# Kernel optimization log

Measured on AMD Instinct MI355X. Metric: run time of the kernel, lower is better.

The kernel has to match this reference:

```python
import jax, jax.numpy as jnp
import numpy as np

C_V, C_F, C_D = 10, 64, 16
COSTS = jnp.array([10.0, 5.0, 2.0], dtype=jnp.float32)  # bandwidth cost per granularity
PENALTY = 0.0  # no_transmission_utility_penalty


def setup_inputs() -> dict:
    key = jax.random.key(0)
    k1, k2 = jax.random.split(key)
    B, H, W = 4, 192, 192
    collab = jax.random.normal(k1, (B, C_V + C_F + C_D, H, W), dtype=jnp.float32)
    utility = jax.random.normal(k2, (B, H, W, 3), dtype=jnp.float32)
    return {"collab_bev_data_list": collab, "utility_map_list": utility,
            "bandwidth_budget": 200000}


def _selection_mechanism(utility, budget_per_sample):
    # utility: [B, H, W, G]; returns [B, H, W] float selected granularity (-1 = none)
    B, H, W, G = utility.shape
    best_u = jnp.max(utility, axis=3)                      # [B,H,W]
    best_g = jnp.argmax(utility, axis=3)                   # [B,H,W]
    N = B * H * W
    flat_u = best_u.reshape(N)
    flat_g = best_g.reshape(N)
    b_idx = jnp.repeat(jnp.arange(B, dtype=jnp.int32), H * W)
    valid = flat_u > PENALTY
    cost = COSTS[flat_g]                                   # [N]
    # sort candidates by utility, descending (stable, matching list.sort)
    order = jnp.argsort(-flat_u)
    v_s = valid[order]
    c_s = cost[order]
    b_s = b_idx[order]

    # greedy budget-constrained selection per sample (sequential knapsack)
    def step(usage, item):
        v, c, b = item
        ok = v & (usage[b] + c <= budget_per_sample)
        usage = usage.at[b].add(jnp.where(ok, c, jnp.float32(0)))
        return usage, ok

    _, sel_sorted = jax.lax.scan(step, jnp.zeros((B,), jnp.float32), (v_s, c_s, b_s))
    selected = jnp.zeros((N,), bool).at[order].set(sel_sorted)
    idx = jnp.where(selected, flat_g.astype(jnp.float32), jnp.float32(-1.0))
    return idx.reshape(B, H, W)


def _build_sparse_bev(sel_idx, vox, feat, det):
    m0 = (sel_idx == 0.0)[:, None, :, :]
    m1 = (sel_idx == 1.0)[:, None, :, :]
    m2 = (sel_idx == 2.0)[:, None, :, :]
    return jnp.concatenate([vox * m0, feat * m1, det * m2], axis=1)


def reference(collab_bev_data_list, utility_map_list, bandwidth_budget):
    cav_num = collab_bev_data_list.shape[0]
    budget_per_sample = jnp.float32(bandwidth_budget / cav_num)
    sel_idx = _selection_mechanism(utility_map_list, budget_per_sample)
    vox = collab_bev_data_list[:, :C_V]
    feat = collab_bev_data_list[:, C_V:C_V + C_F]
    det = collab_bev_data_list[:, C_V + C_F:C_V + C_F + C_D]
    sparse = _build_sparse_bev(sel_idx, vox, feat, det)
    return sparse, sel_idx
```

## Files before the change

kernel.cpp:

```cpp
#include <hip/hip_runtime.h>
#include <stdint.h>
#include <math.h>

#define B_    4
#define H_    192
#define W_    192
#define HW    (H_*W_)
#define NPIX  (B_*HW)
#define C_V   10
#define C_F   64
#define C_D   16
#define C_ALL (C_V+C_F+C_D)
#define HBINS 32768
#define CAP   2048

#define OFF_HIST 0u
#define OFF_KEY  (4u*HBINS*4u)
#define OFF_G    (OFF_KEY + (uint32_t)NPIX*4u)
#define OFF_SELX (OFF_G + (uint32_t)NPIX)
#define OFF_HL   (OFF_SELX + (uint32_t)NPIX)

__device__ __forceinline__ uint32_t costOf(uint32_t g) {
    return g == 0u ? 10u : (g == 1u ? 5u : 2u);
}

__device__ __forceinline__ uint32_t budgetInt(const int* bptr) {
    double bps = (double)bptr[0] / (double)B_;
    float f = (float)bps;
    return (uint32_t)floorf(f);
}

__global__ void k_zero(uint4* __restrict__ hist4) {
    int i = blockIdx.x * blockDim.x + threadIdx.x;
    hist4[i] = make_uint4(0u, 0u, 0u, 0u);
}

__global__ void k_prep(const float* __restrict__ util, uint4* __restrict__ key4,
                       uint32_t* __restrict__ g4, uint32_t* __restrict__ selx4,
                       uint32_t* __restrict__ hist) {
    int t = blockIdx.x * blockDim.x + threadIdx.x;
    if (t >= NPIX / 4) return;
    const float4* u4 = (const float4*)util + (size_t)t * 3;
    float4 a = u4[0], b4 = u4[1], c4 = u4[2];
    float u[4][3] = { {a.x, a.y, a.z}, {a.w, b4.x, b4.y},
                      {b4.z, b4.w, c4.x}, {c4.y, c4.z, c4.w} };
    uint32_t kk[4]; uint32_t gpack = 0;
    #pragma unroll
    for (int p = 0; p < 4; ++p) {
        float best = u[p][0]; uint32_t g = 0;
        if (u[p][1] > best) { best = u[p][1]; g = 1; }
        if (u[p][2] > best) { best = u[p][2]; g = 2; }
        kk[p] = (best > 0.0f) ? (__float_as_uint(best) | 0x80000000u) : 0u;
        gpack |= g << (8 * p);
    }
    key4[t] = make_uint4(kk[0], kk[1], kk[2], kk[3]);
    g4[t] = gpack;
    selx4[t] = 0u;
    int b = (t * 4) / HW;
    #pragma unroll
    for (int p = 0; p < 4; ++p)
        if (kk[p])
            atomicAdd(&hist[(size_t)b * HBINS + ((kk[p] >> 16) & 32767u)],
                      costOf((gpack >> (8 * p)) & 3u));
}

__global__ __launch_bounds__(1024) void k_select(const uint32_t* __restrict__ key,
                                                 const uint8_t* __restrict__ g,
                                                 const uint32_t* __restrict__ hist,
                                                 const int* __restrict__ budget_ptr,
                                                 uint8_t* __restrict__ selx,
                                                 uint32_t* __restrict__ hl_out) {
    int b = blockIdx.x;
    int t = threadIdx.x;
    uint32_t budget = budgetInt(budget_ptr);

    __shared__ uint32_t scan[1024];
    __shared__ uint64_t e[CAP];
    __shared__ uint64_t s[CAP];
    __shared__ uint64_t red[1024];
    __shared__ uint32_t f_b2, f_usage, sh_n, sh_r, sh_poskey, sh_pospix;

    if (t == 0) { f_b2 = 0xFFFFFFFFu; f_usage = 0u; sh_n = 0u; }
    __syncthreads();

    const uint32_t* hb = hist + (size_t)b * HBINS;
    int hi = 32767 - 32 * t;
    uint32_t cs = 0;
    #pragma unroll 4
    for (int j = 0; j < 32; ++j) cs += hb[hi - j];
    scan[t] = cs;
    __syncthreads();
    for (int off = 1; off < 1024; off <<= 1) {
        uint32_t v = (t >= off) ? scan[t - off] : 0u;
        __syncthreads();
        scan[t] += v;
        __syncthreads();
    }
    uint32_t incl = scan[t], excl = incl - cs;
    if (excl <= budget && incl > budget) {
        uint32_t cum = excl;
        for (int j = 0; j < 32; ++j) {
            uint32_t hv = hb[hi - j];
            if (cum + hv > budget) { f_b2 = (uint32_t)(hi - j); f_usage = cum; break; }
            cum += hv;
        }
    }
    __syncthreads();
    uint32_t b2 = f_b2;
    if (t == 0) {
        uint32_t hl;
        if (b2 == 0xFFFFFFFFu)           hl = 1u;
        else {
            uint32_t bs = b2 + 32768u;
            hl = (bs >= 65535u) ? 0xFFFFFFFFu : ((bs + 1u) << 16);
        }
        hl_out[b] = hl;
    }
    if (b2 == 0xFFFFFFFFu) return;

    const uint32_t* kb = key + (size_t)b * HW;
    const uint8_t*  gb = g   + (size_t)b * HW;
    for (int i = t; i < HW; i += 1024) {
        uint32_t k = kb[i];
        if (k && ((k >> 16) & 32767u) == b2) {
            uint32_t idx = atomicAdd(&sh_n, 1u);
            if (idx < CAP)
                e[idx] = ((uint64_t)(~k) << 32) | ((uint64_t)i << 2) | (uint64_t)gb[i];
        }
    }
    __syncthreads();
    int n = (int)(sh_n < (uint32_t)CAP ? sh_n : (uint32_t)CAP);

    for (int i = t; i < n; i += 1024) {
        uint64_t ei = e[i];
        int rk = 0;
        for (int j = 0; j < n; ++j) rk += (e[j] < ei);
        s[rk] = ei;
    }
    __syncthreads();

    if (t == 0) {
        uint32_t usage = f_usage;
        uint8_t* sx = selx + (size_t)b * HW;
        for (int i = 0; i < n; ++i) {
            uint64_t ei = s[i];
            uint32_t c = costOf((uint32_t)(ei & 3u));
            if (usage + c <= budget) { usage += c; sx[(ei >> 2) & 0xFFFFu] = 1; }
        }
        sh_r = budget - usage;
        sh_poskey = (b2 + 32768u) << 16;
        sh_pospix = 0xFFFFFFFFu;
    }
    __syncthreads();

    for (int round = 0; round < 8; ++round) {
        uint32_t r = sh_r;
        if (r < 2u) break;
        uint32_t pkey = sh_poskey, ppix = sh_pospix;
        uint64_t best = 0;
        for (int i = t; i < HW; i += 1024) {
            uint32_t k = kb[i];
            if (!k) continue;
            if (!(k < pkey || (k == pkey && (uint32_t)i > ppix))) continue;
            if (costOf(gb[i]) > r) continue;
            uint64_t m = ((uint64_t)k << 16) | (uint64_t)(65535u - (uint32_t)i);
            if (m > best) best = m;
        }
        red[t] = best;
        __syncthreads();
        for (int off = 512; off > 0; off >>= 1) {
            if (t < off) {
                uint64_t o = red[t + off];
                if (o > red[t]) red[t] = o;
            }
            __syncthreads();
        }
        if (t == 0) {
            uint64_t m = red[0];
            if (m == 0) sh_r = 0;
            else {
                uint32_t pix = 65535u - (uint32_t)(m & 0xFFFFu);
                uint32_t k   = (uint32_t)(m >> 16);
                uint32_t c   = costOf(gb[pix]);
                selx[(size_t)b * HW + pix] = 1;
                sh_r -= c;
                sh_poskey = k; sh_pospix = pix;
            }
        }
        __syncthreads();
    }
}

__global__ void k_sparse(const float* __restrict__ collab, const uint4* __restrict__ key4,
                         const uint32_t* __restrict__ g4, const uint32_t* __restrict__ selx4,
                         const uint32_t* __restrict__ hl_arr,
                         float* __restrict__ out, float* __restrict__ selOut) {
    int tid = blockIdx.x * blockDim.x + threadIdx.x;
    int c = blockIdx.y, b = blockIdx.z;
    int cls = (c < C_V) ? 0 : ((c < C_V + C_F) ? 1 : 2);
    uint32_t hl = hl_arr[b];
    size_t p4 = (size_t)b * (HW / 4) + (size_t)tid;
    uint4 kk = key4[p4];
    uint32_t gg = g4[p4];
    uint32_t sx = selx4[p4];
    int sc[4];
    uint32_t kv[4] = { kk.x, kk.y, kk.z, kk.w };
    #pragma unroll
    for (int p = 0; p < 4; ++p) {
        bool se = (kv[p] >= hl) || (((sx >> (8 * p)) & 0xFFu) != 0u);
        sc[p] = se ? (int)((gg >> (8 * p)) & 3u) : -1;
    }
    size_t co = ((size_t)(b * C_ALL + c)) * HW + (size_t)tid * 4;
    float4 v = *(const float4*)(collab + co);
    float4 o;
    o.x = (sc[0] == cls) ? v.x : 0.0f;
    o.y = (sc[1] == cls) ? v.y : 0.0f;
    o.z = (sc[2] == cls) ? v.z : 0.0f;
    o.w = (sc[3] == cls) ? v.w : 0.0f;
    *(float4*)(out + co) = o;
    if (c == 0) {
        float4 sf = make_float4((float)sc[0], (float)sc[1], (float)sc[2], (float)sc[3]);
        ((float4*)selOut)[p4] = sf;
    }
}

extern "C" void kernel_launch(void* const* d_in, const int* in_sizes, int n_in,
                              void* d_out, int out_size, void* d_ws, size_t ws_size,
                              hipStream_t stream) {
    (void)in_sizes; (void)n_in; (void)out_size; (void)ws_size;
    const float* collab = (const float*)d_in[0];
    const float* util   = (const float*)d_in[1];
    const int*   budget = (const int*)d_in[2];

    uint8_t*  ws   = (uint8_t*)d_ws;
    uint32_t* hist = (uint32_t*)(ws + OFF_HIST);
    uint32_t* key  = (uint32_t*)(ws + OFF_KEY);
    uint8_t*  g    = ws + OFF_G;
    uint8_t*  selx = ws + OFF_SELX;
    uint32_t* hl   = (uint32_t*)(ws + OFF_HL);

    float* outSparse = (float*)d_out;
    float* outSel    = outSparse + (size_t)B_ * C_ALL * HW;

    k_zero  <<<(4 * HBINS / 4) / 256, 256, 0, stream>>>((uint4*)hist);
    k_prep  <<<(NPIX / 4 + 255) / 256, 256, 0, stream>>>(util, (uint4*)key,
                                                         (uint32_t*)g, (uint32_t*)selx, hist);
    k_select<<<B_, 1024, 0, stream>>>(key, g, hist, budget, selx, hl);
    dim3 grid3(HW / 4 / 256, C_ALL, B_);
    k_sparse<<<grid3, 256, 0, stream>>>(collab, (const uint4*)key, (const uint32_t*)g,
                                        (const uint32_t*)selx, hl, outSparse, outSel);
}
```

Measured before the change: 88.91 us.

## Replace iterative tail-fill rounds with single-pass top-k candidates and wavefront-shuffle scan

```diff
diff --git a/kernel.cpp b/kernel.cpp
--- a/kernel.cpp
+++ b/kernel.cpp
@@ -30,6 +30,9 @@
     return (uint32_t)floorf(f);
 }
 
+#define CE(x, y) { uint64_t _mn = (x) < (y) ? (x) : (y); \
+                   uint64_t _mx = (x) < (y) ? (y) : (x); (x) = _mx; (y) = _mn; }
+
 __global__ void k_zero(uint4* __restrict__ hist4) {
     int i = blockIdx.x * blockDim.x + threadIdx.x;
     hist4[i] = make_uint4(0u, 0u, 0u, 0u);
@@ -72,13 +75,16 @@
                                                  uint32_t* __restrict__ hl_out) {
     int b = blockIdx.x;
     int t = threadIdx.x;
+    int lane = t & 63, wv = t >> 6;
     uint32_t budget = budgetInt(budget_ptr);
 
-    __shared__ uint32_t scan[1024];
     __shared__ uint64_t e[CAP];
     __shared__ uint64_t s[CAP];
-    __shared__ uint64_t red[1024];
-    __shared__ uint32_t f_b2, f_usage, sh_n, sh_r, sh_poskey, sh_pospix;
+    __shared__ uint32_t wsum[16];
+    __shared__ uint64_t red5[16];
+    __shared__ uint64_t red2[16][4];
+    __shared__ uint64_t cand[5];
+    __shared__ uint32_t f_b2, f_usage, sh_n, sh_r;
 
     if (t == 0) { f_b2 = 0xFFFFFFFFu; f_usage = 0u; sh_n = 0u; }
     __syncthreads();
@@ -88,15 +94,26 @@
     uint32_t cs = 0;
     #pragma unroll 4
     for (int j = 0; j < 32; ++j) cs += hb[hi - j];
-    scan[t] = cs;
-    __syncthreads();
-    for (int off = 1; off < 1024; off <<= 1) {
-        uint32_t v = (t >= off) ? scan[t - off] : 0u;
-        __syncthreads();
-        scan[t] += v;
-        __syncthreads();
-    }
-    uint32_t incl = scan[t], excl = incl - cs;
+    uint32_t v = cs;
+    #pragma unroll
+    for (int off = 1; off < 64; off <<= 1) {
+        uint32_t o = __shfl_up(v, off);
+        if (lane >= off) v += o;
+    }
+    if (lane == 63) wsum[wv] = v;
+    __syncthreads();
+    if (t < 16) {
+        uint32_t w = wsum[t];
+        #pragma unroll
+        for (int off = 1; off < 16; off <<= 1) {
+            uint32_t o = __shfl_up(w, off);
+            if (t >= off) w += o;
+        }
+        wsum[t] = w;
+    }
+    __syncthreads();
+    uint32_t incl = v + (wv ? wsum[wv - 1] : 0u);
+    uint32_t excl = incl - cs;
     if (excl <= budget && incl > budget) {
         uint32_t cum = excl;
         for (int j = 0; j < 32; ++j) {
@@ -120,13 +137,44 @@
 
     const uint32_t* kb = key + (size_t)b * HW;
     const uint8_t*  gb = g   + (size_t)b * HW;
+    uint64_t m5 = 0;
+    uint64_t a0 = 0, a1 = 0, a2 = 0, a3 = 0;
     for (int i = t; i < HW; i += 1024) {
         uint32_t k = kb[i];
-        if (k && ((k >> 16) & 32767u) == b2) {
+        if (!k) continue;
+        uint32_t bin = (k >> 16) & 32767u;
+        if (bin == b2) {
             uint32_t idx = atomicAdd(&sh_n, 1u);
             if (idx < CAP)
                 e[idx] = ((uint64_t)(~k) << 32) | ((uint64_t)i << 2) | (uint64_t)gb[i];
-        }
+        } else if (bin < b2) {
+            uint32_t gg = gb[i];
+            if (gg == 0u) continue;
+            uint64_t m = ((uint64_t)k << 18) | ((uint64_t)(65535u - (uint32_t)i) << 2)
+                       | (uint64_t)gg;
+            if (gg == 1u) { if (m > m5) m5 = m; }
+            else {
+                if (m > a3) {
+                    if      (m > a0) { a3 = a2; a2 = a1; a1 = a0; a0 = m; }
+                    else if (m > a1) { a3 = a2; a2 = a1; a1 = m; }
+                    else if (m > a2) { a3 = a2; a2 = m; }
+                    else             { a3 = m; }
+                }
+            }
+        }
+    }
+    #pragma unroll
+    for (int off = 32; off; off >>= 1) {
+        uint64_t o5 = __shfl_down(m5, off);
+        if (o5 > m5) m5 = o5;
+        uint64_t b0 = __shfl_down(a0, off), b1 = __shfl_down(a1, off),
+                 b2_ = __shfl_down(a2, off), b3 = __shfl_down(a3, off);
+        CE(a0, b3); CE(a1, b2_); CE(a2, b1); CE(a3, b0);
+        CE(a0, a2); CE(a1, a3); CE(a0, a1); CE(a2, a3);
+    }
+    if (lane == 0) {
+        red5[wv] = m5;
+        red2[wv][0] = a0; red2[wv][1] = a1; red2[wv][2] = a2; red2[wv][3] = a3;
     }
     __syncthreads();
     int n = (int)(sh_n < (uint32_t)CAP ? sh_n : (uint32_t)CAP);
@@ -147,47 +195,38 @@
             uint32_t c = costOf((uint32_t)(ei & 3u));
             if (usage + c <= budget) { usage += c; sx[(ei >> 2) & 0xFFFFu] = 1; }
         }
-        sh_r = budget - usage;
-        sh_poskey = (b2 + 32768u) << 16;
-        sh_pospix = 0xFFFFFFFFu;
-    }
-    __syncthreads();
-
-    for (int round = 0; round < 8; ++round) {
-        uint32_t r = sh_r;
-        if (r < 2u) break;
-        uint32_t pkey = sh_poskey, ppix = sh_pospix;
-        uint64_t best = 0;
-        for (int i = t; i < HW; i += 1024) {
-            uint32_t k = kb[i];
-            if (!k) continue;
-            if (!(k < pkey || (k == pkey && (uint32_t)i > ppix))) continue;
-            if (costOf(gb[i]) > r) continue;
-            uint64_t m = ((uint64_t)k << 16) | (uint64_t)(65535u - (uint32_t)i);
-            if (m > best) best = m;
-        }
-        red[t] = best;
-        __syncthreads();
-        for (int off = 512; off > 0; off >>= 1) {
-            if (t < off) {
-                uint64_t o = red[t + off];
-                if (o > red[t]) red[t] = o;
+        uint64_t g5 = 0, t0 = 0, t1 = 0, t2 = 0, t3 = 0;
+        for (int wq = 0; wq < 16; ++wq) {
+            if (red5[wq] > g5) g5 = red5[wq];
+            #pragma unroll
+            for (int q = 0; q < 4; ++q) {
+                uint64_t m = red2[wq][q];
+                if (m > t3) {
+                    if      (m > t0) { t3 = t2; t2 = t1; t1 = t0; t0 = m; }
+                    else if (m > t1) { t3 = t2; t2 = t1; t1 = m; }
+                    else if (m > t2) { t3 = t2; t2 = m; }
+                    else             { t3 = m; }
+                }
             }
-            __syncthreads();
-        }
-        if (t == 0) {
-            uint64_t m = red[0];
-            if (m == 0) sh_r = 0;
-            else {
-                uint32_t pix = 65535u - (uint32_t)(m & 0xFFFFu);
-                uint32_t k   = (uint32_t)(m >> 16);
-                uint32_t c   = costOf(gb[pix]);
-                selx[(size_t)b * HW + pix] = 1;
-                sh_r -= c;
-                sh_poskey = k; sh_pospix = pix;
+        }
+        cand[0] = g5; cand[1] = t0; cand[2] = t1; cand[3] = t2; cand[4] = t3;
+        for (int i = 1; i < 5; ++i) {
+            uint64_t x = cand[i]; int j = i;
+            while (j > 0 && cand[j - 1] < x) { cand[j] = cand[j - 1]; --j; }
+            cand[j] = x;
+        }
+        uint32_t r = budget - usage;
+        for (int i = 0; i < 5; ++i) {
+            uint64_t m = cand[i];
+            if (!m) break;
+            uint32_t c = costOf((uint32_t)(m & 3u));
+            if (c <= r) {
+                r -= c;
+                uint32_t pix = 65535u - (uint32_t)((m >> 2) & 0xFFFFu);
+                sx[pix] = 1;
             }
         }
-        __syncthreads();
+        sh_r = r; (void)sh_r;
     }
 }
 
```

Measured after the change: 107.5 us. 1.21x slower.
